# Optimization experiments

Measured on AMD Instinct MI355X. Metric: run time of the kernel, lower is better.

The kernel has to match this reference:

```python
import jax, jax.numpy as jnp
import numpy as np

CUTOFF = 5.2
BOX = 44.0
N_ATOMS = 8192

# 13 half-shifts used by the cell list (vector_index_displacement) + zero shift
HALF_SHIFTS = np.array([
    [-1, 0, 0], [-1, -1, 0], [0, -1, 0], [1, -1, 0],
    [-1, 1, -1], [0, 1, -1], [1, 1, -1], [-1, 0, -1],
    [0, 0, -1], [1, 0, -1], [-1, -1, -1], [0, -1, -1], [1, -1, -1]], dtype=np.int64)
ALL_SHIFTS = np.concatenate([np.zeros((1, 3), dtype=np.int64), HALF_SHIFTS], axis=0)  # (14,3)


def setup_inputs() -> dict:
    key = jax.random.key(0)
    k1, k2 = jax.random.split(key)
    species = jax.random.randint(k1, (1, N_ATOMS), 0, 4, dtype=jnp.int64)
    coordinates = jax.random.uniform(k2, (1, N_ATOMS, 3), dtype=jnp.float32) * BOX
    cell = jnp.eye(3, dtype=jnp.float32) * BOX
    pbc = jnp.ones((3,), dtype=bool)
    return {"species": species, "coordinates": coordinates, "cell": cell, "pbc": pbc}


def reference(species, coordinates, cell, pbc):
    # Single molecule, as asserted by the torch module.
    coords = coordinates[0]  # (N, 3)
    n = coords.shape[0]
    # map_to_central: wrap coordinates into the central cell
    frac = coords @ jnp.linalg.inv(cell)
    frac = frac - jnp.floor(frac)
    coords = frac @ cell
    # orthorhombic cell diagonal (norm of cell columns, as in _setup_variables)
    diag = jnp.linalg.norm(cell, axis=0)  # (3,)

    shifts = jnp.asarray(ALL_SHIFTS)
    pairs_list, shift_list = [], []
    cutoff2 = CUTOFF * CUTOFF
    for k in range(shifts.shape[0]):  # fixed small loop over 14 periodic shifts
        s = shifts[k]
        # delta[i, j] = r_i - r_j + s * cell_diagonal   (N, N, 3)
        delta = coords[:, None, :] - coords[None, :, :] + s.astype(coords.dtype) * diag
        d2 = jnp.sum(delta * delta, axis=-1)  # (N, N)
        mask = d2 <= cutoff2
        if k == 0:
            # within-image pairs: each unordered pair once, no self pairs
            mask = jnp.triu(mask, 1)
        i, j = jnp.nonzero(mask)  # eager: data-dependent pair count
        pairs_list.append(jnp.stack([i, j], axis=0))
        shift_list.append(jnp.broadcast_to(s, (i.shape[0], 3)))
    atom_pairs = jnp.concatenate(pairs_list, axis=1)  # (2, P)
    shift_indices = jnp.concatenate(shift_list, axis=0)  # (P, 3)
    return atom_pairs, shift_indices


if __name__ == "__main__":
    out = reference(**setup_inputs())
    print(out[0].shape, out[1].shape)
```

## Files before the change

### kernel.cpp

```cpp
#include <hip/hip_runtime.h>

#define CLJ_NATOMS 8192
#define CLJ_NSHIFT 14
#define CLJ_NROWS (CLJ_NSHIFT * CLJ_NATOMS)
#define CLJ_NTILE 112
#define CLJ_NCELL 512
#define CLJ_CAP 128
#define CLJ_PWAVES 8192
#define CLJ_C2 ((float)(5.2 * 5.2))
#define CLJ_R 5.35f

__device__ const int clj_shifts[CLJ_NSHIFT][3] = {
    {0, 0, 0},
    {-1, 0, 0}, {-1, -1, 0}, {0, -1, 0}, {1, -1, 0},
    {-1, 1, -1}, {0, 1, -1}, {1, 1, -1}, {-1, 0, -1},
    {0, 0, -1}, {1, 0, -1}, {-1, -1, -1}, {0, -1, -1}, {1, -1, -1}};

__device__ float4 clj_pp[CLJ_NATOMS];
__device__ int clj_cid[CLJ_NATOMS];
__device__ float4 clj_sorted[CLJ_NATOMS];
__device__ unsigned clj_cstart[CLJ_NCELL + 1];
__device__ unsigned clj_cfill[CLJ_NCELL];
__device__ unsigned clj_flag;
__device__ unsigned clj_nalive;
__device__ unsigned clj_alist[CLJ_NROWS];
__device__ int clj_jbuf[(size_t)CLJ_NROWS * CLJ_CAP];
__device__ unsigned clj_cnt[CLJ_NROWS];
__device__ unsigned clj_off[CLJ_NROWS];
__device__ unsigned clj_tot[CLJ_NTILE];
__device__ float4 clj_dg;
__device__ float4 clj_cinv;
__device__ float4 clj_sf[CLJ_NSHIFT];

__device__ __forceinline__ bool clj_alive_f(float xi, float yi, float zi, int sx,
                                            int sy, int sz, float dgx, float dgy,
                                            float dgz) {
  bool a = true;
  if (sx < 0) a = a && (xi >= dgx - 5.3f); else if (sx > 0) a = a && (xi <= 5.3f);
  if (sy < 0) a = a && (yi >= dgy - 5.3f); else if (sy > 0) a = a && (yi <= 5.3f);
  if (sz < 0) a = a && (zi >= dgz - 5.3f); else if (sz > 0) a = a && (zi <= 5.3f);
  return a;
}

__device__ __forceinline__ void clj_crange(float t, float ci, int& lo, int& hi) {
  lo = max(0, (int)(fmaxf(t - CLJ_R, 0.f) * ci));
  hi = min(7, (int)(fmaxf(t + CLJ_R, 0.f) * ci));
}

__device__ __forceinline__ unsigned clj_iscan(unsigned v, int lane) {
  for (int off = 1; off < 64; off <<= 1) {
    unsigned t = __shfl_up(v, off);
    if (lane >= off) v += t;
  }
  return v;
}

__global__ __launch_bounds__(256) void clj_wrapbin(const float* __restrict__ coords,
                                                   const float* __restrict__ cell) {
  int i = blockIdx.x * blockDim.x + threadIdx.x;
  if (i >= CLJ_NATOMS) return;
  if (i == 0) {
    clj_flag = 0u;
    clj_nalive = 0u;
  }
#pragma unroll
  for (int k = 0; k < CLJ_NSHIFT; ++k) clj_cnt[(k << 13) + i] = 0u;

  float dgx = (float)sqrt((double)cell[0] * cell[0] + (double)cell[3] * cell[3] +
                          (double)cell[6] * cell[6]);
  float dgy = (float)sqrt((double)cell[1] * cell[1] + (double)cell[4] * cell[4] +
                          (double)cell[7] * cell[7]);
  float dgz = (float)sqrt((double)cell[2] * cell[2] + (double)cell[5] * cell[5] +
                          (double)cell[8] * cell[8]);
  float cix = 8.0f / dgx, ciy = 8.0f / dgy, ciz = 8.0f / dgz;
  if (i == 0) {
    clj_dg = make_float4(dgx, dgy, dgz, 0.f);
    clj_cinv = make_float4(cix, ciy, ciz, 0.f);
    for (int k = 0; k < CLJ_NSHIFT; ++k)
      clj_sf[k] = make_float4(__fmul_rn((float)clj_shifts[k][0], dgx),
                              __fmul_rn((float)clj_shifts[k][1], dgy),
                              __fmul_rn((float)clj_shifts[k][2], dgz), 0.f);
  }

  double a00 = cell[0], a01 = cell[1], a02 = cell[2];
  double a10 = cell[3], a11 = cell[4], a12 = cell[5];
  double a20 = cell[6], a21 = cell[7], a22 = cell[8];
  double det = a00 * (a11 * a22 - a12 * a21) - a01 * (a10 * a22 - a12 * a20) +
               a02 * (a10 * a21 - a11 * a20);
  double id = 1.0 / det;
  float inv[3][3];
  inv[0][0] = (float)((a11 * a22 - a12 * a21) * id);
  inv[0][1] = (float)(-(a01 * a22 - a02 * a21) * id);
  inv[0][2] = (float)((a01 * a12 - a02 * a11) * id);
  inv[1][0] = (float)(-(a10 * a22 - a12 * a20) * id);
  inv[1][1] = (float)((a00 * a22 - a02 * a20) * id);
  inv[1][2] = (float)(-(a00 * a12 - a02 * a10) * id);
  inv[2][0] = (float)((a10 * a21 - a11 * a20) * id);
  inv[2][1] = (float)(-(a00 * a21 - a01 * a20) * id);
  inv[2][2] = (float)((a00 * a11 - a01 * a10) * id);

  float x = coords[3 * i], y = coords[3 * i + 1], z = coords[3 * i + 2];
  float fr[3], w[3];
#pragma unroll
  for (int c = 0; c < 3; ++c) {
    float f = __fadd_rn(__fadd_rn(__fmul_rn(x, inv[0][c]), __fmul_rn(y, inv[1][c])),
                        __fmul_rn(z, inv[2][c]));
    fr[c] = __fsub_rn(f, floorf(f));
  }
#pragma unroll
  for (int c = 0; c < 3; ++c) {
    w[c] = __fadd_rn(
        __fadd_rn(__fmul_rn(fr[0], cell[0 * 3 + c]), __fmul_rn(fr[1], cell[1 * 3 + c])),
        __fmul_rn(fr[2], cell[2 * 3 + c]));
  }
  clj_pp[i] = make_float4(w[0], w[1], w[2], 0.0f);
  int cx = min(7, (int)(w[0] * cix));
  int cy = min(7, (int)(w[1] * ciy));
  int cz = min(7, (int)(w[2] * ciz));
  clj_cid[i] = (cz * 8 + cy) * 8 + cx;
}

__global__ __launch_bounds__(512) void clj_scatterfused() {
  __shared__ unsigned h[CLJ_NCELL];
  int tid = threadIdx.x;
  if (blockIdx.x == 0) {
    h[tid] = 0u;
    __syncthreads();
    for (int r = tid; r < CLJ_NATOMS; r += 512) atomicAdd(&h[clj_cid[r]], 1u);
    __syncthreads();
    unsigned v = h[tid];
    unsigned acc = v;
    for (int off = 1; off < CLJ_NCELL; off <<= 1) {
      unsigned a = (tid >= off) ? h[tid - off] : 0u;
      __syncthreads();
      acc += a;
      h[tid] = acc;
      __syncthreads();
    }
    clj_cstart[tid] = acc - v;
    atomicExch(&clj_cfill[tid], acc - v);
    if (tid == CLJ_NCELL - 1) clj_cstart[CLJ_NCELL] = acc;
    __threadfence();
    __syncthreads();
    if (tid == 0) atomicExch(&clj_flag, 1u);
  } else {
    if (tid == 0) {
      while (atomicAdd(&clj_flag, 0u) == 0u) __builtin_amdgcn_s_sleep(8);
    }
    __syncthreads();
    __threadfence();
  }
  int i = blockIdx.x * 512 + tid;
  float4 p = clj_pp[i];
  unsigned pos = atomicAdd(&clj_cfill[clj_cid[i]], 1u);
  float4 ps = p;
  ps.w = __int_as_float(i);
  clj_sorted[pos] = ps;

  float4 dg = clj_dg;
  unsigned rows[CLJ_NSHIFT];
  int m = 0;
  rows[m++] = (unsigned)i;
#pragma unroll
  for (int k = 1; k < CLJ_NSHIFT; ++k) {
    if (clj_alive_f(p.x, p.y, p.z, clj_shifts[k][0], clj_shifts[k][1],
                    clj_shifts[k][2], dg.x, dg.y, dg.z))
      rows[m++] = (unsigned)((k << 13) + i);
  }
  unsigned base = atomicAdd(&clj_nalive, (unsigned)m);
  for (int q = 0; q < m; ++q) clj_alist[base + q] = rows[q];
}

__global__ __launch_bounds__(512) void clj_count() {
  __shared__ uint4 smask[8][64];
  int wslot = threadIdx.x >> 6;
  int lane = threadIdx.x & 63;
  unsigned* lm = (unsigned*)smask[wslot];
  unsigned na = clj_nalive;
  float4 cinv = clj_cinv;

  for (unsigned w = blockIdx.x * 8 + wslot; w < na; w += CLJ_PWAVES) {
    unsigned row = clj_alist[w];
    int k = row >> 13, i = row & (CLJ_NATOMS - 1);
    float4 sc = clj_sf[k];
    float4 pi = clj_pp[i];
    smask[wslot][lane] = make_uint4(0u, 0u, 0u, 0u);

    int xlo, xhi, ylo, yhi, zlo, zhi;
    clj_crange(__fadd_rn(pi.x, sc.x), cinv.x, xlo, xhi);
    clj_crange(__fadd_rn(pi.y, sc.y), cinv.y, ylo, yhi);
    clj_crange(__fadd_rn(pi.z, sc.z), cinv.z, zlo, zhi);

    for (int cz = zlo; cz <= zhi; ++cz) {
      for (int cy = ylo; cy <= yhi; ++cy) {
        int idb = (cz * 8 + cy) * 8;
        unsigned b = clj_cstart[idb + xlo], e = clj_cstart[idb + xhi + 1];
        for (unsigned t = b + lane; t < e; t += 64) {
          float4 pj = clj_sorted[t];
          int j = __float_as_int(pj.w);
          float dx = __fadd_rn(__fsub_rn(pi.x, pj.x), sc.x);
          float dy = __fadd_rn(__fsub_rn(pi.y, pj.y), sc.y);
          float dz = __fadd_rn(__fsub_rn(pi.z, pj.z), sc.z);
          float d2 = __fadd_rn(__fadd_rn(__fmul_rn(dx, dx), __fmul_rn(dy, dy)),
                               __fmul_rn(dz, dz));
          bool ok = (d2 <= CLJ_C2) && (k != 0 || i < j);
          if (ok) atomicOr(&lm[(unsigned)j >> 5], 1u << (j & 31));
        }
      }
    }
    __threadfence_block();

    const unsigned long long* mrow = (const unsigned long long*)lm;
    unsigned long long m0 = mrow[lane];
    unsigned long long m1 = mrow[64 + lane];
    if (__ballot((m0 | m1) != 0ull) == 0ull) continue;

    unsigned c0 = (unsigned)__popcll(m0), c1 = (unsigned)__popcll(m1);
    unsigned s0 = clj_iscan(c0, lane);
    unsigned T0 = __shfl(s0, 63);
    unsigned e0 = s0 - c0;
    unsigned s1 = clj_iscan(c1, lane);
    unsigned T1 = __shfl(s1, 63);
    unsigned e1 = T0 + s1 - c1;

    size_t jb = (size_t)row * CLJ_CAP;
    unsigned p = e0;
    unsigned long long m = m0;
    while (m) {
      int b = __ffsll((long long)m) - 1;
      m &= m - 1;
      if (p < CLJ_CAP) clj_jbuf[jb + p] = (lane << 6) + b;
      ++p;
    }
    p = e1;
    m = m1;
    while (m) {
      int b = __ffsll((long long)m) - 1;
      m &= m - 1;
      if (p < CLJ_CAP) clj_jbuf[jb + p] = ((64 + lane) << 6) + b;
      ++p;
    }
    if (lane == 0) clj_cnt[row] = min(T0 + T1, (unsigned)CLJ_CAP);
  }
}

__global__ __launch_bounds__(1024) void clj_s1() {
  __shared__ unsigned sd[1024];
  int t = threadIdx.x;
  int gid = blockIdx.x * 1024 + t;
  unsigned v = clj_cnt[gid];
  sd[t] = v;
  __syncthreads();
  unsigned acc = v;
  for (int off = 1; off < 1024; off <<= 1) {
    unsigned a = (t >= off) ? sd[t - off] : 0u;
    __syncthreads();
    acc += a;
    sd[t] = acc;
    __syncthreads();
  }
  clj_off[gid] = acc - v;
  if (t == 1023) clj_tot[blockIdx.x] = acc;
}

__global__ __launch_bounds__(512) void clj_emit(int* __restrict__ out, int P) {
  int wslot = threadIdx.x >> 6;
  int lane = threadIdx.x & 63;
  unsigned na = clj_nalive;

  for (unsigned w = blockIdx.x * 8 + wslot; w < na; w += CLJ_PWAVES) {
    unsigned row = clj_alist[w];
    unsigned c = clj_cnt[row];
    if (c == 0) continue;
    int tile = row >> 10;
    unsigned v = 0;
    if (lane < tile) v = clj_tot[lane];
    if (64 + lane < tile) v += clj_tot[64 + lane];
#pragma unroll
    for (int off = 32; off; off >>= 1) v += __shfl_down(v, off);
    unsigned tbase = __shfl(v, 0);

    unsigned off0 = clj_off[row] + tbase;
    int k = row >> 13, i = row & (CLJ_NATOMS - 1);
    int sx = clj_shifts[k][0], sy = clj_shifts[k][1], sz = clj_shifts[k][2];
    size_t jb = (size_t)row * CLJ_CAP;
    for (unsigned q = lane; q < c; q += 64) {
      unsigned p = off0 + q;
      if (p < (unsigned)P) {
        out[p] = i;
        out[P + p] = clj_jbuf[jb + q];
        unsigned sp = 2u * (unsigned)P + 3u * p;
        out[sp] = sx;
        out[sp + 1] = sy;
        out[sp + 2] = sz;
      }
    }
  }
}

extern "C" void kernel_launch(void* const* d_in, const int* in_sizes, int n_in,
                              void* d_out, int out_size, void* d_ws, size_t ws_size,
                              hipStream_t stream) {
  const float* coords = (const float*)d_in[1];
  const float* cell = (const float*)d_in[2];
  int P = out_size / 5;

  clj_wrapbin<<<CLJ_NATOMS / 256, 256, 0, stream>>>(coords, cell);
  clj_scatterfused<<<16, 512, 0, stream>>>();
  clj_count<<<CLJ_PWAVES / 8, 512, 0, stream>>>();
  clj_s1<<<CLJ_NTILE, 1024, 0, stream>>>();
  clj_emit<<<CLJ_PWAVES / 8, 512, 0, stream>>>((int*)d_out, P);
}
```

Before: 50.70 us.

## Replace spin-wait histogram and separate scan kernel with redundant per-block work

The scatter kernel no longer has block 0 build the cell histogram while the other blocks spin on a global flag. Instead every block recomputes the histogram and its prefix sum redundantly and draws positions from a zeroed per-cell fill counter. The per-row prefix-scan kernel is removed. Count now atomically adds row counts into per-tile totals, and emit computes each row's offset by summing preceding counts within its tile. This drops one launch and the cross-block spin, at the cost of extra histogram work per block and a within-tile reduction per row in emit.

```diff
diff --git a/kernel.cpp b/kernel.cpp
--- a/kernel.cpp
+++ b/kernel.cpp
@@ -1,38 +1,36 @@
 #include <hip/hip_runtime.h>
 
-#define CLJ_NATOMS 8192
-#define CLJ_NSHIFT 14
-#define CLJ_NROWS (CLJ_NSHIFT * CLJ_NATOMS)
-#define CLJ_NTILE 112
-#define CLJ_NCELL 512
-#define CLJ_CAP 128
-#define CLJ_PWAVES 8192
-#define CLJ_C2 ((float)(5.2 * 5.2))
-#define CLJ_R 5.35f
-
-__device__ const int clj_shifts[CLJ_NSHIFT][3] = {
+#define CLN_NATOMS 8192
+#define CLN_NSHIFT 14
+#define CLN_NROWS (CLN_NSHIFT * CLN_NATOMS)
+#define CLN_NTILE 112
+#define CLN_NCELL 512
+#define CLN_CAP 128
+#define CLN_PWAVES 8192
+#define CLN_C2 ((float)(5.2 * 5.2))
+#define CLN_R 5.35f
+
+__device__ const int cln_shifts[CLN_NSHIFT][3] = {
     {0, 0, 0},
     {-1, 0, 0}, {-1, -1, 0}, {0, -1, 0}, {1, -1, 0},
     {-1, 1, -1}, {0, 1, -1}, {1, 1, -1}, {-1, 0, -1},
     {0, 0, -1}, {1, 0, -1}, {-1, -1, -1}, {0, -1, -1}, {1, -1, -1}};
 
-__device__ float4 clj_pp[CLJ_NATOMS];
-__device__ int clj_cid[CLJ_NATOMS];
-__device__ float4 clj_sorted[CLJ_NATOMS];
-__device__ unsigned clj_cstart[CLJ_NCELL + 1];
-__device__ unsigned clj_cfill[CLJ_NCELL];
-__device__ unsigned clj_flag;
-__device__ unsigned clj_nalive;
-__device__ unsigned clj_alist[CLJ_NROWS];
-__device__ int clj_jbuf[(size_t)CLJ_NROWS * CLJ_CAP];
-__device__ unsigned clj_cnt[CLJ_NROWS];
-__device__ unsigned clj_off[CLJ_NROWS];
-__device__ unsigned clj_tot[CLJ_NTILE];
-__device__ float4 clj_dg;
-__device__ float4 clj_cinv;
-__device__ float4 clj_sf[CLJ_NSHIFT];
-
-__device__ __forceinline__ bool clj_alive_f(float xi, float yi, float zi, int sx,
+__device__ float4 cln_pp[CLN_NATOMS];
+__device__ int cln_cid[CLN_NATOMS];
+__device__ float4 cln_sorted[CLN_NATOMS];
+__device__ unsigned cln_cstart[CLN_NCELL + 1];
+__device__ unsigned cln_cfill0[CLN_NCELL];
+__device__ unsigned cln_nalive;
+__device__ unsigned cln_alist[CLN_NROWS];
+__device__ int cln_jbuf[(size_t)CLN_NROWS * CLN_CAP];
+__device__ unsigned cln_cnt[CLN_NROWS];
+__device__ unsigned cln_tot[CLN_NTILE];
+__device__ float4 cln_dg;
+__device__ float4 cln_cinv;
+__device__ float4 cln_sf[CLN_NSHIFT];
+
+__device__ __forceinline__ bool cln_alive_f(float xi, float yi, float zi, int sx,
                                             int sy, int sz, float dgx, float dgy,
                                             float dgz) {
   bool a = true;
@@ -42,12 +40,12 @@
   return a;
 }
 
-__device__ __forceinline__ void clj_crange(float t, float ci, int& lo, int& hi) {
-  lo = max(0, (int)(fmaxf(t - CLJ_R, 0.f) * ci));
-  hi = min(7, (int)(fmaxf(t + CLJ_R, 0.f) * ci));
-}
-
-__device__ __forceinline__ unsigned clj_iscan(unsigned v, int lane) {
+__device__ __forceinline__ void cln_crange(float t, float ci, int& lo, int& hi) {
+  lo = max(0, (int)(fmaxf(t - CLN_R, 0.f) * ci));
+  hi = min(7, (int)(fmaxf(t + CLN_R, 0.f) * ci));
+}
+
+__device__ __forceinline__ unsigned cln_iscan(unsigned v, int lane) {
   for (int off = 1; off < 64; off <<= 1) {
     unsigned t = __shfl_up(v, off);
     if (lane >= off) v += t;
@@ -55,16 +53,15 @@
   return v;
 }
 
-__global__ __launch_bounds__(256) void clj_wrapbin(const float* __restrict__ coords,
+__global__ __launch_bounds__(256) void cln_wrapbin(const float* __restrict__ coords,
                                                    const float* __restrict__ cell) {
   int i = blockIdx.x * blockDim.x + threadIdx.x;
-  if (i >= CLJ_NATOMS) return;
-  if (i == 0) {
-    clj_flag = 0u;
-    clj_nalive = 0u;
-  }
-#pragma unroll
-  for (int k = 0; k < CLJ_NSHIFT; ++k) clj_cnt[(k << 13) + i] = 0u;
+  if (i >= CLN_NATOMS) return;
+  if (i < CLN_NTILE) cln_tot[i] = 0u;
+  if (i < CLN_NCELL) cln_cfill0[i] = 0u;
+  if (i == 0) cln_nalive = 0u;
+#pragma unroll
+  for (int k = 0; k < CLN_NSHIFT; ++k) cln_cnt[(k << 13) + i] = 0u;
 
   float dgx = (float)sqrt((double)cell[0] * cell[0] + (double)cell[3] * cell[3] +
                           (double)cell[6] * cell[6]);
@@ -74,12 +71,12 @@
                           (double)cell[8] * cell[8]);
   float cix = 8.0f / dgx, ciy = 8.0f / dgy, ciz = 8.0f / dgz;
   if (i == 0) {
-    clj_dg = make_float4(dgx, dgy, dgz, 0.f);
-    clj_cinv = make_float4(cix, ciy, ciz, 0.f);
-    for (int k = 0; k < CLJ_NSHIFT; ++k)
-      clj_sf[k] = make_float4(__fmul_rn((float)clj_shifts[k][0], dgx),
-                              __fmul_rn((float)clj_shifts[k][1], dgy),
-                              __fmul_rn((float)clj_shifts[k][2], dgz), 0.f);
+    cln_dg = make_float4(dgx, dgy, dgz, 0.f);
+    cln_cinv = make_float4(cix, ciy, ciz, 0.f);
+    for (int k = 0; k < CLN_NSHIFT; ++k)
+      cln_sf[k] = make_float4(__fmul_rn((float)cln_shifts[k][0], dgx),
+                              __fmul_rn((float)cln_shifts[k][1], dgy),
+                              __fmul_rn((float)cln_shifts[k][2], dgz), 0.f);
   }
 
   double a00 = cell[0], a01 = cell[1], a02 = cell[2];
@@ -113,97 +110,93 @@
         __fadd_rn(__fmul_rn(fr[0], cell[0 * 3 + c]), __fmul_rn(fr[1], cell[1 * 3 + c])),
         __fmul_rn(fr[2], cell[2 * 3 + c]));
   }
-  clj_pp[i] = make_float4(w[0], w[1], w[2], 0.0f);
+  cln_pp[i] = make_float4(w[0], w[1], w[2], 0.0f);
   int cx = min(7, (int)(w[0] * cix));
   int cy = min(7, (int)(w[1] * ciy));
   int cz = min(7, (int)(w[2] * ciz));
-  clj_cid[i] = (cz * 8 + cy) * 8 + cx;
-}
-
-__global__ __launch_bounds__(512) void clj_scatterfused() {
-  __shared__ unsigned h[CLJ_NCELL];
+  cln_cid[i] = (cz * 8 + cy) * 8 + cx;
+}
+
+__global__ __launch_bounds__(512) void cln_scatter() {
+  __shared__ unsigned h[CLN_NCELL];
+  __shared__ unsigned sc[CLN_NCELL];
   int tid = threadIdx.x;
+  h[tid] = 0u;
+  __syncthreads();
+#pragma unroll
+  for (int r = 0; r < 16; ++r) atomicAdd(&h[cln_cid[tid + r * 512]], 1u);
+  __syncthreads();
+  unsigned v = h[tid];
+  unsigned acc = v;
+  for (int off = 1; off < CLN_NCELL; off <<= 1) {
+    unsigned a = (tid >= off) ? h[tid - off] : 0u;
+    __syncthreads();
+    acc += a;
+    h[tid] = acc;
+    __syncthreads();
+  }
+  sc[tid] = acc - v;
   if (blockIdx.x == 0) {
-    h[tid] = 0u;
-    __syncthreads();
-    for (int r = tid; r < CLJ_NATOMS; r += 512) atomicAdd(&h[clj_cid[r]], 1u);
-    __syncthreads();
-    unsigned v = h[tid];
-    unsigned acc = v;
-    for (int off = 1; off < CLJ_NCELL; off <<= 1) {
-      unsigned a = (tid >= off) ? h[tid - off] : 0u;
-      __syncthreads();
-      acc += a;
-      h[tid] = acc;
-      __syncthreads();
-    }
-    clj_cstart[tid] = acc - v;
-    atomicExch(&clj_cfill[tid], acc - v);
-    if (tid == CLJ_NCELL - 1) clj_cstart[CLJ_NCELL] = acc;
-    __threadfence();
-    __syncthreads();
-    if (tid == 0) atomicExch(&clj_flag, 1u);
-  } else {
-    if (tid == 0) {
-      while (atomicAdd(&clj_flag, 0u) == 0u) __builtin_amdgcn_s_sleep(8);
-    }
-    __syncthreads();
-    __threadfence();
-  }
+    cln_cstart[tid] = acc - v;
+    if (tid == CLN_NCELL - 1) cln_cstart[CLN_NCELL] = acc;
+  }
+  __syncthreads();
+
   int i = blockIdx.x * 512 + tid;
-  float4 p = clj_pp[i];
-  unsigned pos = atomicAdd(&clj_cfill[clj_cid[i]], 1u);
+  float4 p = cln_pp[i];
+  int c = cln_cid[i];
+  unsigned pos = sc[c] + atomicAdd(&cln_cfill0[c], 1u);
   float4 ps = p;
   ps.w = __int_as_float(i);
-  clj_sorted[pos] = ps;
-
-  float4 dg = clj_dg;
-  unsigned rows[CLJ_NSHIFT];
+  cln_sorted[pos] = ps;
+
+  float4 dg = cln_dg;
+  unsigned rows[CLN_NSHIFT];
   int m = 0;
   rows[m++] = (unsigned)i;
 #pragma unroll
-  for (int k = 1; k < CLJ_NSHIFT; ++k) {
-    if (clj_alive_f(p.x, p.y, p.z, clj_shifts[k][0], clj_shifts[k][1],
-                    clj_shifts[k][2], dg.x, dg.y, dg.z))
+  for (int k = 1; k < CLN_NSHIFT; ++k) {
+    if (cln_alive_f(p.x, p.y, p.z, cln_shifts[k][0], cln_shifts[k][1],
+                    cln_shifts[k][2], dg.x, dg.y, dg.z))
       rows[m++] = (unsigned)((k << 13) + i);
   }
-  unsigned base = atomicAdd(&clj_nalive, (unsigned)m);
-  for (int q = 0; q < m; ++q) clj_alist[base + q] = rows[q];
-}
-
-__global__ __launch_bounds__(512) void clj_count() {
+  unsigned base = atomicAdd(&cln_nalive, (unsigned)m);
+  for (int q = 0; q < m; ++q) cln_alist[base + q] = rows[q];
+}
+
+__global__ __launch_bounds__(512) void cln_count() {
   __shared__ uint4 smask[8][64];
   int wslot = threadIdx.x >> 6;
   int lane = threadIdx.x & 63;
   unsigned* lm = (unsigned*)smask[wslot];
-  unsigned na = clj_nalive;
-  float4 cinv = clj_cinv;
-
-  for (unsigned w = blockIdx.x * 8 + wslot; w < na; w += CLJ_PWAVES) {
-    unsigned row = clj_alist[w];
-    int k = row >> 13, i = row & (CLJ_NATOMS - 1);
-    float4 sc = clj_sf[k];
-    float4 pi = clj_pp[i];
+  unsigned na = cln_nalive;
+  float4 cinv = cln_cinv;
+
+  for (unsigned w = blockIdx.x * 8 + wslot; w < na; w += CLN_PWAVES) {
+    unsigned row = cln_alist[w];
+    int k = row >> 13, i = row & (CLN_NATOMS - 1);
+    float4 sc = cln_sf[k];
+    float4 pi = cln_pp[i];
     smask[wslot][lane] = make_uint4(0u, 0u, 0u, 0u);
 
     int xlo, xhi, ylo, yhi, zlo, zhi;
-    clj_crange(__fadd_rn(pi.x, sc.x), cinv.x, xlo, xhi);
-    clj_crange(__fadd_rn(pi.y, sc.y), cinv.y, ylo, yhi);
-    clj_crange(__fadd_rn(pi.z, sc.z), cinv.z, zlo, zhi);
+    cln_crange(__fadd_rn(pi.x, sc.x), cinv.x, xlo, xhi);
+    cln_crange(__fadd_rn(pi.y, sc.y), cinv.y, ylo, yhi);
+    cln_crange(__fadd_rn(pi.z, sc.z), cinv.z, zlo, zhi);
 
     for (int cz = zlo; cz <= zhi; ++cz) {
       for (int cy = ylo; cy <= yhi; ++cy) {
         int idb = (cz * 8 + cy) * 8;
-        unsigned b = clj_cstart[idb + xlo], e = clj_cstart[idb + xhi + 1];
+        unsigned b = cln_cstart[idb + xlo], e = cln_cstart[idb + xhi + 1];
         for (unsigned t = b + lane; t < e; t += 64) {
-          float4 pj = clj_sorted[t];
+          float4 pj = cln_sorted[t];
           int j = __float_as_int(pj.w);
           float dx = __fadd_rn(__fsub_rn(pi.x, pj.x), sc.x);
           float dy = __fadd_rn(__fsub_rn(pi.y, pj.y), sc.y);
           float dz = __fadd_rn(__fsub_rn(pi.z, pj.z), sc.z);
           float d2 = __fadd_rn(__fadd_rn(__fmul_rn(dx, dx), __fmul_rn(dy, dy)),
                                __fmul_rn(dz, dz));
-          bool ok = (d2 <= CLJ_C2) && (k != 0 || i < j);
+          bool ok = (d2 <= CLN_C2) && (k != 0 || i < j);
           if (ok) atomicOr(&lm[(unsigned)j >> 5], 1u << (j & 31));
         }
       }
@@ -216,20 +209,20 @@
     if (__ballot((m0 | m1) != 0ull) == 0ull) continue;
 
     unsigned c0 = (unsigned)__popcll(m0), c1 = (unsigned)__popcll(m1);
-    unsigned s0 = clj_iscan(c0, lane);
+    unsigned s0 = cln_iscan(c0, lane);
     unsigned T0 = __shfl(s0, 63);
     unsigned e0 = s0 - c0;
-    unsigned s1 = clj_iscan(c1, lane);
+    unsigned s1 = cln_iscan(c1, lane);
     unsigned T1 = __shfl(s1, 63);
     unsigned e1 = T0 + s1 - c1;
 
-    size_t jb = (size_t)row * CLJ_CAP;
+    size_t jb = (size_t)row * CLN_CAP;
     unsigned p = e0;
     unsigned long long m = m0;
     while (m) {
       int b = __ffsll((long long)m) - 1;
       m &= m - 1;
-      if (p < CLJ_CAP) clj_jbuf[jb + p] = (lane << 6) + b;
+      if (p < CLN_CAP) cln_jbuf[jb + p] = (lane << 6) + b;
       ++p;
     }
     p = e1;
@@ -237,58 +230,46 @@
     while (m) {
       int b = __ffsll((long long)m) - 1;
       m &= m - 1;
-      if (p < CLJ_CAP) clj_jbuf[jb + p] = ((64 + lane) << 6) + b;
+      if (p < CLN_CAP) cln_jbuf[jb + p] = ((64 + lane) << 6) + b;
       ++p;
     }
-    if (lane == 0) clj_cnt[row] = min(T0 + T1, (unsigned)CLJ_CAP);
-  }
-}
-
-__global__ __launch_bounds__(1024) void clj_s1() {
-  __shared__ unsigned sd[1024];
-  int t = threadIdx.x;
-  int gid = blockIdx.x * 1024 + t;
-  unsigned v = clj_cnt[gid];
-  sd[t] = v;
-  __syncthreads();
-  unsigned acc = v;
-  for (int off = 1; off < 1024; off <<= 1) {
-    unsigned a = (t >= off) ? sd[t - off] : 0u;
-    __syncthreads();
-    acc += a;
-    sd[t] = acc;
-    __syncthreads();
-  }
-  clj_off[gid] = acc - v;
-  if (t == 1023) clj_tot[blockIdx.x] = acc;
-}
-
-__global__ __launch_bounds__(512) void clj_emit(int* __restrict__ out, int P) {
+    if (lane == 0) {
+      unsigned cv = min(T0 + T1, (unsigned)CLN_CAP);
+      cln_cnt[row] = cv;
+      atomicAdd(&cln_tot[row >> 10], cv);
+    }
+  }
+}
+
+__global__ __launch_bounds__(512) void cln_emit(int* __restrict__ out, int P) {
   int wslot = threadIdx.x >> 6;
   int lane = threadIdx.x & 63;
-  unsigned na = clj_nalive;
-
-  for (unsigned w = blockIdx.x * 8 + wslot; w < na; w += CLJ_PWAVES) {
-    unsigned row = clj_alist[w];
-    unsigned c = clj_cnt[row];
+  unsigned na = cln_nalive;
+
+  for (unsigned w = blockIdx.x * 8 + wslot; w < na; w += CLN_PWAVES) {
+    unsigned row = cln_alist[w];
+    unsigned c = cln_cnt[row];
     if (c == 0) continue;
-    int tile = row >> 10;
+    int tile = (int)(row >> 10);
+    unsigned tb = (unsigned)tile << 10;
+    unsigned local = row & 1023u;
+
     unsigned v = 0;
-    if (lane < tile) v = clj_tot[lane];
-    if (64 + lane < tile) v += clj_tot[64 + lane];
+    if (lane < tile) v = cln_tot[lane];
+    if (64 + lane < tile) v += cln_tot[64 + lane];
+    for (unsigned q = lane; q < local; q += 64) v += cln_cnt[tb + q];
 #pragma unroll
     for (int off = 32; off; off >>= 1) v += __shfl_down(v, off);
-    unsigned tbase = __shfl(v, 0);
-
-    unsigned off0 = clj_off[row] + tbase;
-    int k = row >> 13, i = row & (CLJ_NATOMS - 1);
-    int sx = clj_shifts[k][0], sy = clj_shifts[k][1], sz = clj_shifts[k][2];
-    size_t jb = (size_t)row * CLJ_CAP;
+    unsigned off0 = __shfl(v, 0);
+
+    int k = row >> 13, i = row & (CLN_NATOMS - 1);
+    int sx = cln_shifts[k][0], sy = cln_shifts[k][1], sz = cln_shifts[k][2];
+    size_t jb = (size_t)row * CLN_CAP;
     for (unsigned q = lane; q < c; q += 64) {
       unsigned p = off0 + q;
       if (p < (unsigned)P) {
         out[p] = i;
-        out[P + p] = clj_jbuf[jb + q];
+        out[P + p] = cln_jbuf[jb + q];
         unsigned sp = 2u * (unsigned)P + 3u * p;
         out[sp] = sx;
         out[sp + 1] = sy;
@@ -305,9 +286,8 @@
   const float* cell = (const float*)d_in[2];
   int P = out_size / 5;
 
-  clj_wrapbin<<<CLJ_NATOMS / 256, 256, 0, stream>>>(coords, cell);
-  clj_scatterfused<<<16, 512, 0, stream>>>();
-  clj_count<<<CLJ_PWAVES / 8, 512, 0, stream>>>();
-  clj_s1<<<CLJ_NTILE, 1024, 0, stream>>>();
-  clj_emit<<<CLJ_PWAVES / 8, 512, 0, stream>>>((int*)d_out, P);
-}
+  cln_wrapbin<<<CLN_NATOMS / 256, 256, 0, stream>>>(coords, cell);
+  cln_scatter<<<16, 512, 0, stream>>>();
+  cln_count<<<CLN_PWAVES / 8, 512, 0, stream>>>();
+  cln_emit<<<CLN_PWAVES / 8, 512, 0, stream>>>((int*)d_out, P);
+}
```

Result: slower. 135.7 us (+167.6%).
